# Kernel optimization log

Hardware: AMD Instinct MI355X
Metric: run time of the kernel (lower is better)

The kernel has to match this reference:

```python
import jax, jax.numpy as jnp
import numpy as np

CAPACITY_FACTOR = 1.25  # config.capacity_factor


def setup_inputs() -> dict:
    key = jax.random.key(0)
    ks = jax.random.split(key, 5)
    B, S, D, F, E = 8, 2048, 768, 3072, 8
    return {
        "x": jax.random.normal(ks[0], (B, S, D), jnp.float32),
        "switch_w": jax.random.normal(ks[1], (D, E), jnp.float32) * 0.02,
        "switch_b": jnp.zeros((E,), jnp.float32),
        "w1": jax.random.normal(ks[2], (E, D, F), jnp.float32) * 0.02,
        "b1": jnp.zeros((E, F), jnp.float32),
        "w2": jax.random.normal(ks[3], (E, F, D), jnp.float32) * 0.02,
        "b2": jnp.zeros((E, D), jnp.float32),
    }


def reference(x, switch_w, switch_b, w1, b1, w2, b2):
    B, S, D = x.shape
    E = w1.shape[0]
    xf = x.reshape(-1, D)                      # [N, D] tokens
    N = xf.shape[0]
    capacity = int(CAPACITY_FACTOR * N / E)

    # top-1 switch routing
    probs = jax.nn.softmax(xf @ switch_w + switch_b, axis=-1)   # [N, E]
    prob_max = jnp.max(probs, axis=-1)                          # [N]
    routes = jnp.argmax(probs, axis=-1)                         # [N] int

    # priority drop: within each expert keep the `capacity` tokens with
    # highest gate prob. Rank tokens within their expert by descending prob.
    sort_idx = jnp.lexsort((-prob_max, routes))                 # [N]
    counts = jnp.bincount(routes, length=E)
    starts = jnp.concatenate([jnp.zeros((1,), counts.dtype), jnp.cumsum(counts)[:-1]])
    rank_sorted = jnp.arange(N) - starts[routes[sort_idx]]
    rank = jnp.zeros((N,), jnp.int32).at[sort_idx].set(rank_sorted.astype(jnp.int32))
    keep = rank < capacity

    # dispatch kept tokens into [E, capacity, D]; overflow goes to slot E
    dest_e = jnp.where(keep, routes, E)
    dest_c = jnp.where(keep, rank, 0)
    buf = jnp.zeros((E + 1, capacity, D), xf.dtype).at[dest_e, dest_c].set(xf)

    # per-expert FFN (grouped GEMM), GELU is exact (erf) as in nn.GELU()
    h = jax.nn.gelu(jnp.einsum('ecd,edf->ecf', buf[:E], w1) + b1[:, None, :],
                    approximate=False)
    o = jnp.einsum('ecf,efd->ecd', h, w2) + b2[:, None, :]      # [E, cap, D]

    # combine: kept tokens get expert output, dropped tokens pass through x
    y_exp = o[routes, dest_c]                                    # [N, D]
    y = jnp.where(keep[:, None], y_exp, xf)
    out = y * prob_max[:, None]                                  # is_scale_prob
    return out.reshape(B, S, D)
```

## Files before the change

kernel.cpp:

```cpp
#include <hip/hip_runtime.h>
#include <cstdint>
#include <cstddef>

#define E_ 8
#define D_ 768
#define F_ 3072
#define N_ 16384
#define CAP_ 2560
#define NCHUNK_ (N_ / 256)

typedef __attribute__((ext_vector_type(8))) short bf16x8;
typedef __attribute__((ext_vector_type(4))) float f32x4;

__device__ __forceinline__ unsigned short f2bf(float f) {
  unsigned u = __float_as_uint(f);
  u += 0x7fffu + ((u >> 16) & 1u);
  return (unsigned short)(u >> 16);
}

__device__ __forceinline__ void gload16(const void* g, void* l) {
  __builtin_amdgcn_global_load_lds(
      (const __attribute__((address_space(1))) void*)g,
      (__attribute__((address_space(3))) void*)l, 16, 0, 0);
}

__global__ void tcast_kernel(const float* __restrict__ src, unsigned short* __restrict__ dst,
                             int R, int C) {
  __shared__ float tile[64][65];
  int e = blockIdx.z;
  const float* s = src + (size_t)e * R * C;
  unsigned short* d = dst + (size_t)e * R * C;
  int c0 = blockIdx.x * 64, r0 = blockIdx.y * 64;
  int tx = threadIdx.x, ty = threadIdx.y;
  #pragma unroll
  for (int rr = ty; rr < 64; rr += 8) {
    tile[rr][tx]      = s[(size_t)(r0 + rr) * C + c0 + tx];
    tile[rr][tx + 32] = s[(size_t)(r0 + rr) * C + c0 + tx + 32];
  }
  __syncthreads();
  #pragma unroll
  for (int cc = ty; cc < 64; cc += 8) {
    ushort2 o;
    o.x = f2bf(tile[2 * tx][cc]);
    o.y = f2bf(tile[2 * tx + 1][cc]);
    *(ushort2*)&d[(size_t)(c0 + cc) * R + r0 + 2 * tx] = o;
  }
}

__global__ __launch_bounds__(256) void router_kernel(
    const float* __restrict__ x, const float* __restrict__ sw, const float* __restrict__ sb,
    int* __restrict__ route, float* __restrict__ prob,
    unsigned short* __restrict__ xb) {
  __shared__ float wl[E_ * D_];
  int tid = threadIdx.x;
  #pragma unroll
  for (int ee = 0; ee < E_; ++ee)
    for (int dd = tid; dd < D_; dd += 256)
      wl[ee * D_ + dd] = sw[dd * E_ + ee];
  __syncthreads();
  int wave = tid >> 6, lane = tid & 63;
  int tbase = blockIdx.x * 16 + wave * 4;
  #pragma unroll
  for (int tt = 0; tt < 4; ++tt) {
    int t = tbase + tt;
    const float* xp = x + (size_t)t * D_;
    unsigned short* xbp = xb + (size_t)t * D_;
    float acc[E_];
    #pragma unroll
    for (int e = 0; e < E_; ++e) acc[e] = 0.f;
    #pragma unroll
    for (int r = 0; r < D_ / 64; ++r) {
      int dd = r * 64 + lane;
      float xv = xp[dd];
      xbp[dd] = f2bf(xv);
      #pragma unroll
      for (int e = 0; e < E_; ++e) acc[e] += xv * wl[e * D_ + dd];
    }
    #pragma unroll
    for (int e = 0; e < E_; ++e) {
      #pragma unroll
      for (int o = 32; o > 0; o >>= 1) acc[e] += __shfl_xor(acc[e], o);
    }
    if (lane == 0) {
      float mx = -1e30f; int arg = 0;
      #pragma unroll
      for (int e = 0; e < E_; ++e) {
        float l = acc[e] + sb[e];
        acc[e] = l;
        if (l > mx) { mx = l; arg = e; }
      }
      float s = 0.f;
      #pragma unroll
      for (int e = 0; e < E_; ++e) s += expf(acc[e] - mx);
      route[t] = arg;
      prob[t] = 1.f / s;
    }
  }
}

__global__ void hist_kernel(const int* __restrict__ route, int* __restrict__ chunk_hist) {
  __shared__ int h[E_];
  int tid = threadIdx.x;
  if (tid < E_) h[tid] = 0;
  __syncthreads();
  atomicAdd(&h[route[blockIdx.x * 256 + tid]], 1);
  __syncthreads();
  if (tid < E_) chunk_hist[blockIdx.x * E_ + tid] = h[tid];
}

__global__ void scan_kernel(const int* __restrict__ chunk_hist, int* __restrict__ chunk_off,
                            int* __restrict__ counts) {
  __shared__ int h[NCHUNK_ * E_];
  int tid = threadIdx.x;
  h[tid] = chunk_hist[tid];
  __syncthreads();
  if (tid < E_) {
    int run = 0;
    for (int c = 0; c < NCHUNK_; ++c) {
      chunk_off[c * E_ + tid] = run;
      run += h[c * E_ + tid];
    }
    counts[tid] = run;
  }
}

__global__ void assign_kernel(const int* __restrict__ route, const float* __restrict__ prob,
                              const int* __restrict__ counts, const int* __restrict__ chunk_off,
                              int* __restrict__ tok_list, int* __restrict__ slot) {
  __shared__ int rt[256];
  int tid = threadIdx.x;
  int i = blockIdx.x * 256 + tid;
  int e = route[i];
  rt[tid] = e;
  __syncthreads();
  int r = 0;
  for (int j = 0; j < tid; ++j) r += (rt[j] == e) ? 1 : 0;
  int c = counts[e];
  int s; bool keep;
  if (c <= CAP_) {
    s = chunk_off[blockIdx.x * E_ + e] + r;
    keep = true;
  } else {
    float p = prob[i];
    int rr = 0;
    for (int j = 0; j < N_; ++j) {
      if (route[j] == e) {
        float pj = prob[j];
        rr += (pj > p || (pj == p && j < i)) ? 1 : 0;
      }
    }
    s = rr; keep = (rr < CAP_);
  }
  if (keep) tok_list[e * CAP_ + s] = i;
  slot[i] = keep ? s : -1;
}

__global__ __launch_bounds__(256) void gemm1_kernel(
    const unsigned short* __restrict__ xb, const unsigned short* __restrict__ w1t,
    const float* __restrict__ b1, const int* __restrict__ tok_list,
    const int* __restrict__ counts, unsigned short* __restrict__ hb) {
  int e = blockIdx.z;
  int Me = counts[e] < CAP_ ? counts[e] : CAP_;
  int m0 = blockIdx.x * 128;
  if (m0 >= Me) return;
  int n0 = blockIdx.y * 128;
  __shared__ unsigned short At[128 * 32];
  __shared__ unsigned short Bt[128 * 32];
  int tid = threadIdx.x, lane = tid & 63, wave = tid >> 6;
  int rA0 = (wave * 2 + 0) * 16 + (lane >> 2);
  int rA1 = (wave * 2 + 1) * 16 + (lane >> 2);
  int cb = (lane & 3) * 16;
  int mr0 = m0 + rA0; if (mr0 > Me - 1) mr0 = Me - 1;
  int mr1 = m0 + rA1; if (mr1 > Me - 1) mr1 = Me - 1;
  int tok0 = tok_list[e * CAP_ + mr0];
  int tok1 = tok_list[e * CAP_ + mr1];
  const char* gA0 = (const char*)(xb + (size_t)tok0 * D_) + cb;
  const char* gA1 = (const char*)(xb + (size_t)tok1 * D_) + cb;
  const char* gB0 = (const char*)(w1t + ((size_t)e * F_ + n0 + rA0) * D_) + cb;
  const char* gB1 = (const char*)(w1t + ((size_t)e * F_ + n0 + rA1) * D_) + cb;
  unsigned short* lA0 = At + (wave * 2 + 0) * 512;
  unsigned short* lA1 = At + (wave * 2 + 1) * 512;
  unsigned short* lB0 = Bt + (wave * 2 + 0) * 512;
  unsigned short* lB1 = Bt + (wave * 2 + 1) * 512;
  f32x4 acc[4][4] = {};
  int wm = (wave >> 1) * 64, wn = (wave & 1) * 64;
  int fr = lane & 15, fk = (lane >> 4) * 8;
  for (int k0 = 0; k0 < D_; k0 += 32) {
    __syncthreads();
    gload16(gA0 + (size_t)2 * k0, lA0);
    gload16(gA1 + (size_t)2 * k0, lA1);
    gload16(gB0 + (size_t)2 * k0, lB0);
    gload16(gB1 + (size_t)2 * k0, lB1);
    __syncthreads();
    bf16x8 a[4], b[4];
    #pragma unroll
    for (int i = 0; i < 4; ++i)
      a[i] = *(const bf16x8*)(At + (wm + i * 16 + fr) * 32 + fk);
    #pragma unroll
    for (int j = 0; j < 4; ++j)
      b[j] = *(const bf16x8*)(Bt + (wn + j * 16 + fr) * 32 + fk);
    #pragma unroll
    for (int i = 0; i < 4; ++i)
      #pragma unroll
      for (int j = 0; j < 4; ++j)
        acc[i][j] = __builtin_amdgcn_mfma_f32_16x16x32_bf16(a[i], b[j], acc[i][j], 0, 0, 0);
  }
  int q4 = (lane >> 4) * 4;
  #pragma unroll
  for (int i = 0; i < 4; ++i) {
    #pragma unroll
    for (int j = 0; j < 4; ++j) {
      int col = n0 + wn + j * 16 + (lane & 15);
      float bias = b1[e * F_ + col];
      #pragma unroll
      for (int r = 0; r < 4; ++r) {
        int row = m0 + wm + i * 16 + q4 + r;
        if (row < Me) {
          float v = acc[i][j][r] + bias;
          v = 0.5f * v * (1.f + erff(v * 0.70710678118654752f));
          hb[((size_t)e * CAP_ + row) * F_ + col] = f2bf(v);
        }
      }
    }
  }
}

__global__ __launch_bounds__(256) void gemm2_kernel(
    const unsigned short* __restrict__ hb, const unsigned short* __restrict__ w2t,
    const float* __restrict__ b2, const int* __restrict__ tok_list,
    const int* __restrict__ counts, const float* __restrict__ prob,
    float* __restrict__ out) {
  int e = blockIdx.z;
  int Me = counts[e] < CAP_ ? counts[e] : CAP_;
  int m0 = blockIdx.x * 128;
  if (m0 >= Me) return;
  int n0 = blockIdx.y * 128;
  __shared__ unsigned short At[128 * 32];
  __shared__ unsigned short Bt[128 * 32];
  int tid = threadIdx.x, lane = tid & 63, wave = tid >> 6;
  int rA0 = (wave * 2 + 0) * 16 + (lane >> 2);
  int rA1 = (wave * 2 + 1) * 16 + (lane >> 2);
  int cb = (lane & 3) * 16;
  const char* gA0 = (const char*)(hb + ((size_t)e * CAP_ + m0 + rA0) * F_) + cb;
  const char* gA1 = (const char*)(hb + ((size_t)e * CAP_ + m0 + rA1) * F_) + cb;
  const char* gB0 = (const char*)(w2t + ((size_t)e * D_ + n0 + rA0) * F_) + cb;
  const char* gB1 = (const char*)(w2t + ((size_t)e * D_ + n0 + rA1) * F_) + cb;
  unsigned short* lA0 = At + (wave * 2 + 0) * 512;
  unsigned short* lA1 = At + (wave * 2 + 1) * 512;
  unsigned short* lB0 = Bt + (wave * 2 + 0) * 512;
  unsigned short* lB1 = Bt + (wave * 2 + 1) * 512;
  f32x4 acc[4][4] = {};
  int wm = (wave >> 1) * 64, wn = (wave & 1) * 64;
  int fr = lane & 15, fk = (lane >> 4) * 8;
  for (int k0 = 0; k0 < F_; k0 += 32) {
    __syncthreads();
    gload16(gA0 + (size_t)2 * k0, lA0);
    gload16(gA1 + (size_t)2 * k0, lA1);
    gload16(gB0 + (size_t)2 * k0, lB0);
    gload16(gB1 + (size_t)2 * k0, lB1);
    __syncthreads();
    bf16x8 a[4], b[4];
    #pragma unroll
    for (int i = 0; i < 4; ++i)
      a[i] = *(const bf16x8*)(At + (wm + i * 16 + fr) * 32 + fk);
    #pragma unroll
    for (int j = 0; j < 4; ++j)
      b[j] = *(const bf16x8*)(Bt + (wn + j * 16 + fr) * 32 + fk);
    #pragma unroll
    for (int i = 0; i < 4; ++i)
      #pragma unroll
      for (int j = 0; j < 4; ++j)
        acc[i][j] = __builtin_amdgcn_mfma_f32_16x16x32_bf16(a[i], b[j], acc[i][j], 0, 0, 0);
  }
  int q4 = (lane >> 4) * 4;
  #pragma unroll
  for (int i = 0; i < 4; ++i) {
    #pragma unroll
    for (int r = 0; r < 4; ++r) {
      int row = m0 + wm + i * 16 + q4 + r;
      if (row < Me) {
        int tok = tok_list[e * CAP_ + row];
        float pm = prob[tok];
        #pragma unroll
        for (int j = 0; j < 4; ++j) {
          int col = n0 + wn + j * 16 + (lane & 15);
          float v = (acc[i][j][r] + b2[e * D_ + col]) * pm;
          out[(size_t)tok * D_ + col] = v;
        }
      }
    }
  }
}

__global__ void passthrough_kernel(const float* __restrict__ x, const float* __restrict__ prob,
                                   const int* __restrict__ slot, float* __restrict__ out) {
  int t = blockIdx.x;
  if (slot[t] >= 0) return;
  float p = prob[t];
  for (int d = threadIdx.x; d < D_; d += 256)
    out[(size_t)t * D_ + d] = x[(size_t)t * D_ + d] * p;
}

extern "C" void kernel_launch(void* const* d_in, const int* in_sizes, int n_in,
                              void* d_out, int out_size, void* d_ws, size_t ws_size,
                              hipStream_t stream) {
  const float* x  = (const float*)d_in[0];
  const float* sw = (const float*)d_in[1];
  const float* sb = (const float*)d_in[2];
  const float* w1 = (const float*)d_in[3];
  const float* b1 = (const float*)d_in[4];
  const float* w2 = (const float*)d_in[5];
  const float* b2 = (const float*)d_in[6];
  float* out = (float*)d_out;
  (void)in_sizes; (void)n_in; (void)out_size; (void)ws_size;

  char* ws = (char*)d_ws;
  size_t off = 0;
  auto alloc = [&](size_t bytes) {
    char* p = ws + off;
    off = (off + bytes + 255) & ~(size_t)255;
    return p;
  };
  int* counts     = (int*)alloc(32 * sizeof(int));
  int* chunk_hist = (int*)alloc((size_t)NCHUNK_ * E_ * sizeof(int));
  int* chunk_off  = (int*)alloc((size_t)NCHUNK_ * E_ * sizeof(int));
  int* tok_list   = (int*)alloc((size_t)E_ * CAP_ * sizeof(int));
  int* route      = (int*)alloc((size_t)N_ * 4);
  float* prob     = (float*)alloc((size_t)N_ * 4);
  int* slot       = (int*)alloc((size_t)N_ * 4);
  unsigned short* xb  = (unsigned short*)alloc((size_t)N_ * D_ * 2);
  unsigned short* w1t = (unsigned short*)alloc((size_t)E_ * D_ * F_ * 2);
  unsigned short* w2t = (unsigned short*)alloc((size_t)E_ * D_ * F_ * 2);
  unsigned short* hb  = (unsigned short*)alloc((size_t)E_ * CAP_ * F_ * 2);

  dim3 tb(32, 8);
  tcast_kernel<<<dim3(F_ / 64, D_ / 64, E_), tb, 0, stream>>>(w1, w1t, D_, F_);
  tcast_kernel<<<dim3(D_ / 64, F_ / 64, E_), tb, 0, stream>>>(w2, w2t, F_, D_);
  router_kernel<<<N_ / 16, 256, 0, stream>>>(x, sw, sb, route, prob, xb);
  hist_kernel<<<NCHUNK_, 256, 0, stream>>>(route, chunk_hist);
  scan_kernel<<<1, NCHUNK_ * E_, 0, stream>>>(chunk_hist, chunk_off, counts);
  assign_kernel<<<NCHUNK_, 256, 0, stream>>>(route, prob, counts, chunk_off, tok_list, slot);
  gemm1_kernel<<<dim3(CAP_ / 128, F_ / 128, E_), 256, 0, stream>>>(xb, w1t, b1, tok_list, counts, hb);
  gemm2_kernel<<<dim3(CAP_ / 128, D_ / 128, E_), 256, 0, stream>>>(hb, w2t, b2, tok_list, counts, prob, out);
  passthrough_kernel<<<N_, 256, 0, stream>>>(x, prob, slot, out);
}
```

Before: 590.4 us.

## Retile second expert GEMM to 256x256 double-buffered tiles, swizzle LDS, vectorize transpose stores

The second grouped GEMM moves from 128x128 tiles with 256 threads to 256x256 tiles with 512 threads and a 64-wide K step. It double-buffers LDS with async global-to-LDS loads, XOR-swizzles the LDS layout and raises wave priority around the MFMA block. This is meant to raise operand reuse, hide load latency and avoid bank conflicts. The first GEMM gets the same XOR swizzle on its LDS chunks, and the weight transpose-cast kernel now writes 4 bf16 values per store instead of 2. The cost is 128KB of LDS per block and fewer blocks in flight, which leaves part of the GPU idle for this grid.

New measurement: 539.0 us. -8.7%, faster.

```diff
diff --git a/kernel.cpp b/kernel.cpp
--- a/kernel.cpp
+++ b/kernel.cpp
@@ -38,12 +38,17 @@
     tile[rr][tx + 32] = s[(size_t)(r0 + rr) * C + c0 + tx + 32];
   }
   __syncthreads();
-  #pragma unroll
-  for (int cc = ty; cc < 64; cc += 8) {
-    ushort2 o;
-    o.x = f2bf(tile[2 * tx][cc]);
-    o.y = f2bf(tile[2 * tx + 1][cc]);
-    *(ushort2*)&d[(size_t)(c0 + cc) * R + r0 + 2 * tx] = o;
+  int rr = 4 * (tx & 15);
+  int ccb = (tx >> 4) + 2 * ty;
+  #pragma unroll
+  for (int m = 0; m < 4; ++m) {
+    int cc = ccb + 16 * m;
+    ushort4 o;
+    o.x = f2bf(tile[rr + 0][cc]);
+    o.y = f2bf(tile[rr + 1][cc]);
+    o.z = f2bf(tile[rr + 2][cc]);
+    o.w = f2bf(tile[rr + 3][cc]);
+    *(ushort4*)&d[(size_t)(c0 + cc) * R + r0 + rr] = o;
   }
 }
 
@@ -169,7 +174,7 @@
   int tid = threadIdx.x, lane = tid & 63, wave = tid >> 6;
   int rA0 = (wave * 2 + 0) * 16 + (lane >> 2);
   int rA1 = (wave * 2 + 1) * 16 + (lane >> 2);
-  int cb = (lane & 3) * 16;
+  int cb = (((lane & 3) ^ ((lane >> 2) & 3))) * 16;
   int mr0 = m0 + rA0; if (mr0 > Me - 1) mr0 = Me - 1;
   int mr1 = m0 + rA1; if (mr1 > Me - 1) mr1 = Me - 1;
   int tok0 = tok_list[e * CAP_ + mr0];
@@ -184,7 +189,8 @@
   unsigned short* lB1 = Bt + (wave * 2 + 1) * 512;
   f32x4 acc[4][4] = {};
   int wm = (wave >> 1) * 64, wn = (wave & 1) * 64;
-  int fr = lane & 15, fk = (lane >> 4) * 8;
+  int fr = lane & 15;
+  int fk = (((lane >> 4) ^ (lane & 3))) * 8;
   for (int k0 = 0; k0 < D_; k0 += 32) {
     __syncthreads();
     gload16(gA0 + (size_t)2 * k0, lA0);
@@ -225,56 +231,79 @@
   }
 }
 
-__global__ __launch_bounds__(256) void gemm2_kernel(
+__global__ __launch_bounds__(512, 2) void gemm2_kernel(
     const unsigned short* __restrict__ hb, const unsigned short* __restrict__ w2t,
     const float* __restrict__ b2, const int* __restrict__ tok_list,
     const int* __restrict__ counts, const float* __restrict__ prob,
     float* __restrict__ out) {
   int e = blockIdx.z;
   int Me = counts[e] < CAP_ ? counts[e] : CAP_;
-  int m0 = blockIdx.x * 128;
+  int m0 = blockIdx.x * 256;
   if (m0 >= Me) return;
-  int n0 = blockIdx.y * 128;
-  __shared__ unsigned short At[128 * 32];
-  __shared__ unsigned short Bt[128 * 32];
-  int tid = threadIdx.x, lane = tid & 63, wave = tid >> 6;
-  int rA0 = (wave * 2 + 0) * 16 + (lane >> 2);
-  int rA1 = (wave * 2 + 1) * 16 + (lane >> 2);
-  int cb = (lane & 3) * 16;
-  const char* gA0 = (const char*)(hb + ((size_t)e * CAP_ + m0 + rA0) * F_) + cb;
-  const char* gA1 = (const char*)(hb + ((size_t)e * CAP_ + m0 + rA1) * F_) + cb;
-  const char* gB0 = (const char*)(w2t + ((size_t)e * D_ + n0 + rA0) * F_) + cb;
-  const char* gB1 = (const char*)(w2t + ((size_t)e * D_ + n0 + rA1) * F_) + cb;
-  unsigned short* lA0 = At + (wave * 2 + 0) * 512;
-  unsigned short* lA1 = At + (wave * 2 + 1) * 512;
-  unsigned short* lB0 = Bt + (wave * 2 + 0) * 512;
-  unsigned short* lB1 = Bt + (wave * 2 + 1) * 512;
-  f32x4 acc[4][4] = {};
-  int wm = (wave >> 1) * 64, wn = (wave & 1) * 64;
-  int fr = lane & 15, fk = (lane >> 4) * 8;
-  for (int k0 = 0; k0 < F_; k0 += 32) {
+  int n0 = blockIdx.y * 256;
+  __shared__ unsigned short sm[65536];
+  int tid = threadIdx.x, lane = tid & 63, w = tid >> 6;
+  int srow = w * 8 + (lane >> 3);
+  int schunk = (lane & 7) ^ (lane >> 3);
+  unsigned dstA = (unsigned)(w * 512);
+  const char* sA[4];
+  #pragma unroll
+  for (int ar = 0; ar < 4; ++ar)
+    sA[ar] = (const char*)(hb + ((size_t)e * CAP_ + m0 + ar * 64 + srow) * F_) + schunk * 16;
+  const char* sB = (const char*)(w2t + ((size_t)e * D_ + n0 + srow) * F_) + schunk * 16;
+  const size_t BR = (size_t)64 * F_ * 2;
+  int fr = lane & 15, q = lane >> 4;
+  int wm = (w >> 2) * 128, wn = (w & 3) * 64;
+  f32x4 acc[8][4] = {};
+
+  #pragma unroll
+  for (int ar = 0; ar < 4; ++ar) {
+    gload16(sA[ar], sm + ar * 4096 + dstA);
+    gload16(sB + ar * BR, sm + 16384 + ar * 4096 + dstA);
+  }
+  __syncthreads();
+
+  const int NT = F_ / 64;
+  for (int kt = 0; kt < NT; ++kt) {
+    int cb = kt & 1;
+    if (kt + 1 < NT) {
+      int ob = cb ^ 1;
+      size_t ko = (size_t)(kt + 1) * 128;
+      #pragma unroll
+      for (int ar = 0; ar < 4; ++ar) {
+        gload16(sA[ar] + ko, sm + ob * 32768 + ar * 4096 + dstA);
+        gload16(sB + ar * BR + ko, sm + ob * 32768 + 16384 + ar * 4096 + dstA);
+      }
+    }
+    const unsigned short* A  = sm + cb * 32768;
+    const unsigned short* Bm = A + 16384;
+    #pragma unroll
+    for (int kh = 0; kh < 2; ++kh) {
+      bf16x8 bfr[4];
+      #pragma unroll
+      for (int j = 0; j < 4; ++j) {
+        int row = wn + j * 16 + fr;
+        int pc = (kh * 4 + q) ^ (fr & 7);
+        bfr[j] = *(const bf16x8*)(Bm + row * 64 + pc * 8);
+      }
+      __builtin_amdgcn_s_setprio(1);
+      #pragma unroll
+      for (int i = 0; i < 8; ++i) {
+        int row = wm + i * 16 + fr;
+        int pc = (kh * 4 + q) ^ (fr & 7);
+        bf16x8 afr = *(const bf16x8*)(A + row * 64 + pc * 8);
+        #pragma unroll
+        for (int j = 0; j < 4; ++j)
+          acc[i][j] = __builtin_amdgcn_mfma_f32_16x16x32_bf16(afr, bfr[j], acc[i][j], 0, 0, 0);
+      }
+      __builtin_amdgcn_s_setprio(0);
+    }
     __syncthreads();
-    gload16(gA0 + (size_t)2 * k0, lA0);
-    gload16(gA1 + (size_t)2 * k0, lA1);
-    gload16(gB0 + (size_t)2 * k0, lB0);
-    gload16(gB1 + (size_t)2 * k0, lB1);
-    __syncthreads();
-    bf16x8 a[4], b[4];
-    #pragma unroll
-    for (int i = 0; i < 4; ++i)
-      a[i] = *(const bf16x8*)(At + (wm + i * 16 + fr) * 32 + fk);
-    #pragma unroll
-    for (int j = 0; j < 4; ++j)
-      b[j] = *(const bf16x8*)(Bt + (wn + j * 16 + fr) * 32 + fk);
-    #pragma unroll
-    for (int i = 0; i < 4; ++i)
-      #pragma unroll
-      for (int j = 0; j < 4; ++j)
-        acc[i][j] = __builtin_amdgcn_mfma_f32_16x16x32_bf16(a[i], b[j], acc[i][j], 0, 0, 0);
-  }
-  int q4 = (lane >> 4) * 4;
-  #pragma unroll
-  for (int i = 0; i < 4; ++i) {
+  }
+
+  int q4 = q * 4;
+  #pragma unroll
+  for (int i = 0; i < 8; ++i) {
     #pragma unroll
     for (int r = 0; r < 4; ++r) {
       int row = m0 + wm + i * 16 + q4 + r;
@@ -283,7 +312,7 @@
         float pm = prob[tok];
         #pragma unroll
         for (int j = 0; j < 4; ++j) {
-          int col = n0 + wn + j * 16 + (lane & 15);
+          int col = n0 + wn + j * 16 + fr;
           float v = (acc[i][j][r] + b2[e * D_ + col]) * pm;
           out[(size_t)tok * D_ + col] = v;
         }
@@ -341,6 +370,6 @@
   scan_kernel<<<1, NCHUNK_ * E_, 0, stream>>>(chunk_hist, chunk_off, counts);
   assign_kernel<<<NCHUNK_, 256, 0, stream>>>(route, prob, counts, chunk_off, tok_list, slot);
   gemm1_kernel<<<dim3(CAP_ / 128, F_ / 128, E_), 256, 0, stream>>>(xb, w1t, b1, tok_list, counts, hb);
-  gemm2_kernel<<<dim3(CAP_ / 128, D_ / 128, E_), 256, 0, stream>>>(hb, w2t, b2, tok_list, counts, prob, out);
+  gemm2_kernel<<<dim3(CAP_ / 256, D_ / 256, E_), 512, 0, stream>>>(hb, w2t, b2, tok_list, counts, prob, out);
   passthrough_kernel<<<N_, 256, 0, stream>>>(x, prob, slot, out);
 }
```
